# Kernel optimization log

Measured on AMD Instinct MI355X. Metric: run time of the kernel, lower is better.

Reference implementation:

```python
import jax, jax.numpy as jnp
import numpy as np
import math

H = 80; W = 80
FOVX = math.pi / 2.0; FOVY = math.pi / 2.0
TANX = math.tan(FOVX * 0.5); TANY = math.tan(FOVY * 0.5)
FOCAL_X = W / (2.0 * TANX); FOCAL_Y = H / (2.0 * TANY)
SCALE_MOD = 1.0
N_GAUSS = 4096; K_GEOM = 1024; K_SH = 1024

SH_C0 = 0.28209479177387814
SH_C1 = 0.4886025119029199
C2 = [1.0925484305920792, -1.0925484305920792, 0.31539156525252005, -1.0925484305920792, 0.5462742152960396]
C3 = [-0.5900435899266435, 2.890611442640554, -0.4570457994644658, 0.3731763325901154, -0.4570457994644658, 1.445305721320277, -0.5900435899266435]


def eval_sh3(sh, d):
    # sh: [N,16,3], d: [N,3] unit view directions -> clamped RGB [N,3]
    x, y, z = d[:, 0:1], d[:, 1:2], d[:, 2:3]
    xx, yy, zz = x * x, y * y, z * z
    xy, yz, xz = x * y, y * z, x * z
    res = (SH_C0 * sh[:, 0]
           - SH_C1 * y * sh[:, 1] + SH_C1 * z * sh[:, 2] - SH_C1 * x * sh[:, 3]
           + C2[0] * xy * sh[:, 4] + C2[1] * yz * sh[:, 5]
           + C2[2] * (2.0 * zz - xx - yy) * sh[:, 6]
           + C2[3] * xz * sh[:, 7] + C2[4] * (xx - yy) * sh[:, 8]
           + C3[0] * y * (3.0 * xx - yy) * sh[:, 9] + C3[1] * xy * z * sh[:, 10]
           + C3[2] * y * (4.0 * zz - xx - yy) * sh[:, 11]
           + C3[3] * z * (2.0 * zz - 3.0 * xx - 3.0 * yy) * sh[:, 12]
           + C3[4] * x * (4.0 * zz - xx - yy) * sh[:, 13]
           + C3[5] * z * (xx - yy) * sh[:, 14]
           + C3[6] * x * (xx - yy - 3.0 * zz) * sh[:, 15])
    return jnp.maximum(res + 0.5, 0.0)


def quat_to_rotmat(q):
    # q: [N,4] normalized (w,x,y,z) -> [N,3,3]
    w, x, y, z = q[:, 0], q[:, 1], q[:, 2], q[:, 3]
    r0 = jnp.stack([1 - 2 * (y * y + z * z), 2 * (x * y - w * z), 2 * (x * z + w * y)], -1)
    r1 = jnp.stack([2 * (x * y + w * z), 1 - 2 * (x * x + z * z), 2 * (y * z - w * x)], -1)
    r2 = jnp.stack([2 * (x * z - w * y), 2 * (y * z + w * x), 1 - 2 * (x * x + y * y)], -1)
    return jnp.stack([r0, r1, r2], axis=1)


def _forward(means3D, sh, sh_indices, g_indices, opacities, scales, scale_factors, rotations, extrinsic, bg):
    N = means3D.shape[0]
    # row-vector convention as in the torch wrapper: p_hom = [x,y,z,1] @ view
    R3 = extrinsic[:3, :3]; t3 = extrinsic[3, :3]
    p_view = means3D @ R3 + t3  # [N,3] camera space
    tx, ty, tz = p_view[:, 0], p_view[:, 1], p_view[:, 2]
    in_front = tz > 0.2  # near-plane cull as in CUDA kernel
    tz_s = jnp.where(in_front, tz, 1.0)
    # NDC (projection matrix reduces to x/(z tanx), y/(z tany)) then ndc2Pix
    gx = ((tx / (tz_s * TANX) + 1.0) * W - 1.0) * 0.5
    gy = ((ty / (tz_s * TANY) + 1.0) * H - 1.0) * 0.5
    # indexed 3D covariance: Sigma = R diag(s^2) R^T, codebook gathers
    s = scales[g_indices] * scale_factors * SCALE_MOD  # [N,3]
    q = rotations[g_indices]
    q = q / jnp.linalg.norm(q, axis=1, keepdims=True)
    Rm = quat_to_rotmat(q)
    cov3D = jnp.einsum('nij,nj,nkj->nik', Rm, s * s, Rm)
    # EWA splat: world->cam rotation is R3^T under row-vector storage
    Wm = R3.T
    cov_cam = jnp.einsum('ij,njk,lk->nil', Wm, cov3D, Wm)
    limx = 1.3 * TANX; limy = 1.3 * TANY
    txc = jnp.clip(tx / tz_s, -limx, limx) * tz_s
    tyc = jnp.clip(ty / tz_s, -limy, limy) * tz_s
    J = jnp.zeros((N, 2, 3), means3D.dtype)
    J = J.at[:, 0, 0].set(FOCAL_X / tz_s).at[:, 0, 2].set(-FOCAL_X * txc / (tz_s * tz_s))
    J = J.at[:, 1, 1].set(FOCAL_Y / tz_s).at[:, 1, 2].set(-FOCAL_Y * tyc / (tz_s * tz_s))
    cov2d = jnp.einsum('nij,njk,nlk->nil', J, cov_cam, J)
    a = cov2d[:, 0, 0] + 0.3; b = cov2d[:, 0, 1]; c = cov2d[:, 1, 1] + 0.3
    det = a * c - b * b
    valid = in_front & (det > 0)
    det_s = jnp.where(det != 0, det, 1.0)
    ca = c / det_s; cb = -b / det_s; cc = a / det_s  # conic
    mid = 0.5 * (a + c)
    lam1 = mid + jnp.sqrt(jnp.maximum(0.1, mid * mid - det))
    radii = jnp.where(valid, jnp.ceil(3.0 * jnp.sqrt(lam1)), 0.0).astype(jnp.int32)
    # SH -> RGB, view dir from camera position (extrinsic.inverse()[3,:3])
    campos = jnp.linalg.inv(extrinsic)[3, :3]
    dirs = means3D - campos
    dirs = dirs / jnp.linalg.norm(dirs, axis=1, keepdims=True)
    color = eval_sh3(sh[sh_indices], dirs)  # [N,3]
    # global front-to-back depth sort
    depth = jnp.where(valid, tz, jnp.inf)
    order = jnp.argsort(depth)
    gx_s, gy_s = gx[order], gy[order]
    ca_s, cb_s, cc_s = ca[order], cb[order], cc[order]
    op_s = opacities[order, 0]; col_s = color[order]; val_s = valid[order]
    # pixel grid (pixel centers at integer coords as in renderCUDA)
    ys, xs = jnp.meshgrid(jnp.arange(H, dtype=means3D.dtype), jnp.arange(W, dtype=means3D.dtype), indexing='ij')
    px = xs.reshape(-1); py = ys.reshape(-1)  # [P]
    dx = gx_s[None, :] - px[:, None]  # [P,N]
    dy = gy_s[None, :] - py[:, None]
    power = -0.5 * (ca_s * dx * dx + cc_s * dy * dy) - cb_s * dx * dy
    alpha = jnp.minimum(0.99, op_s[None, :] * jnp.exp(jnp.minimum(power, 0.0)))
    keep = (power <= 0.0) & val_s[None, :] & (alpha >= 1.0 / 255.0)
    alpha = jnp.where(keep, alpha, 0.0)
    om = 1.0 - alpha
    T_inc = jnp.cumprod(om, axis=1)
    inc = T_inc >= 1e-4  # early-termination prefix (T monotone)
    T_excl = jnp.concatenate([jnp.ones((px.shape[0], 1), om.dtype), T_inc[:, :-1]], axis=1)
    w = alpha * T_excl * inc
    T_final = jnp.prod(jnp.where(inc, om, 1.0), axis=1)
    out = w @ col_s + T_final[:, None] * bg[None, :]  # [P,3]
    color_img = jnp.transpose(out.reshape(H, W, 3), (2, 0, 1))  # [3,H,W]
    return color_img, radii


def setup_inputs() -> dict:
    key = jax.random.key(0)
    ks = jax.random.split(key, 9)
    xy = (jax.random.uniform(ks[0], (N_GAUSS, 2)) - 0.5) * 4.0
    z = jax.random.uniform(ks[1], (N_GAUSS, 1)) * 4.0 + 2.0
    means3D = jnp.concatenate([xy, z], axis=1)  # inside the view frustum
    sh = jax.random.normal(ks[2], (K_SH, 16, 3)) * 0.3
    sh_indices = jax.random.randint(ks[3], (N_GAUSS,), 0, K_SH)
    g_indices = jax.random.randint(ks[4], (N_GAUSS,), 0, K_GEOM)
    opacities = jax.random.uniform(ks[5], (N_GAUSS, 1), minval=0.1, maxval=0.99)
    scales = jax.random.uniform(ks[6], (K_GEOM, 3), minval=0.01, maxval=0.08)
    scale_factors = jax.random.uniform(ks[7], (N_GAUSS, 1), minval=0.5, maxval=1.5)
    rotations = jax.random.normal(ks[8], (K_GEOM, 4))
    extrinsic = jnp.eye(4, dtype=jnp.float32)
    bg = jnp.zeros((3,), jnp.float32)
    return dict(means3D=means3D, sh=sh, sh_indices=sh_indices, g_indices=g_indices,
                opacities=opacities, scales=scales, scale_factors=scale_factors,
                rotations=rotations, extrinsic=extrinsic, bg=bg)


def reference(means3D, sh, sh_indices, g_indices, opacities, scales, scale_factors, rotations, extrinsic, bg):
    return _forward(means3D, sh, sh_indices, g_indices, opacities, scales, scale_factors, rotations, extrinsic, bg)
```

## Files before the change

### kernel.cpp

```cpp
#include <hip/hip_runtime.h>
#include <math.h>

#define NG 4096
#define WI 80
#define HI 80
#define NPIX (WI*HI)
#define FOCAL 40.0f
#define LIM 1.3f
#define CAP 1536

#define SH_C0 0.28209479177387814f
#define SH_C1 0.4886025119029199f

#define U0_OFF 0
#define U1_OFF (64*1024)
#define U2_OFF (128*1024)
#define S0_OFF (192*1024)
#define B1_OFF (256*1024)
#define B2_OFF (320*1024)
#define B3_OFF (384*1024)
#define KD_OFF (400*1024)
#define RK_OFF (432*1024)

__global__ __launch_bounds__(256) void prep_k(
    const float* __restrict__ means, const float* __restrict__ sh,
    const int* __restrict__ shidx, const int* __restrict__ gidx,
    const float* __restrict__ opac, const float* __restrict__ scales,
    const float* __restrict__ sfac, const float* __restrict__ rots,
    const float* __restrict__ ext, char* __restrict__ wsb,
    float* __restrict__ radii_out)
{
  int i = blockIdx.x*blockDim.x + threadIdx.x;
  if (i >= NG) return;
  float e0=ext[0],  e1=ext[1],  e2=ext[2];
  float e4=ext[4],  e5=ext[5],  e6=ext[6];
  float e8=ext[8],  e9=ext[9],  e10=ext[10];
  float e12=ext[12], e13=ext[13], e14=ext[14];
  float m0=means[3*i+0], m1=means[3*i+1], m2=means[3*i+2];
  float tx = m0*e0 + m1*e4 + m2*e8  + e12;
  float ty = m0*e1 + m1*e5 + m2*e9  + e13;
  float tz = m0*e2 + m1*e6 + m2*e10 + e14;
  bool infront = tz > 0.2f;
  float tzs = infront ? tz : 1.0f;
  float inv_tzs = 1.0f / tzs;
  float gx = ((tx*inv_tzs + 1.0f)*WI - 1.0f)*0.5f;
  float gy = ((ty*inv_tzs + 1.0f)*HI - 1.0f)*0.5f;

  int gi = gidx[i];
  float sf = sfac[i];
  float s0 = scales[3*gi+0]*sf, s1 = scales[3*gi+1]*sf, s2 = scales[3*gi+2]*sf;
  float qw = rots[4*gi+0], qx = rots[4*gi+1], qy = rots[4*gi+2], qz = rots[4*gi+3];
  float qinv = rsqrtf(qw*qw+qx*qx+qy*qy+qz*qz);
  qw*=qinv; qx*=qinv; qy*=qinv; qz*=qinv;
  float r00 = 1.0f - 2.0f*(qy*qy+qz*qz);
  float r01 = 2.0f*(qx*qy - qw*qz);
  float r02 = 2.0f*(qx*qz + qw*qy);
  float r10 = 2.0f*(qx*qy + qw*qz);
  float r11 = 1.0f - 2.0f*(qx*qx+qz*qz);
  float r12 = 2.0f*(qy*qz - qw*qx);
  float r20 = 2.0f*(qx*qz - qw*qy);
  float r21 = 2.0f*(qy*qz + qw*qx);
  float r22 = 1.0f - 2.0f*(qx*qx+qy*qy);
  float v0 = s0*s0, v1 = s1*s1, v2 = s2*s2;
  float C00 = r00*r00*v0 + r01*r01*v1 + r02*r02*v2;
  float C01 = r00*r10*v0 + r01*r11*v1 + r02*r12*v2;
  float C02 = r00*r20*v0 + r01*r21*v1 + r02*r22*v2;
  float C11 = r10*r10*v0 + r11*r11*v1 + r12*r12*v2;
  float C12 = r10*r20*v0 + r11*r21*v1 + r12*r22*v2;
  float C22 = r20*r20*v0 + r21*r21*v1 + r22*r22*v2;
  float W0x=e0, W0y=e4, W0z=e8;
  float W1x=e1, W1y=e5, W1z=e9;
  float W2x=e2, W2y=e6, W2z=e10;
  float B00 = W0x*C00 + W0y*C01 + W0z*C02;
  float B01 = W0x*C01 + W0y*C11 + W0z*C12;
  float B02 = W0x*C02 + W0y*C12 + W0z*C22;
  float B10 = W1x*C00 + W1y*C01 + W1z*C02;
  float B11 = W1x*C01 + W1y*C11 + W1z*C12;
  float B12 = W1x*C02 + W1y*C12 + W1z*C22;
  float B20 = W2x*C00 + W2y*C01 + W2z*C02;
  float B21 = W2x*C01 + W2y*C11 + W2z*C12;
  float B22 = W2x*C02 + W2y*C12 + W2z*C22;
  float V00 = B00*W0x + B01*W0y + B02*W0z;
  float V02 = B00*W2x + B01*W2y + B02*W2z;
  float V01 = B00*W1x + B01*W1y + B02*W1z;
  float V11 = B10*W1x + B11*W1y + B12*W1z;
  float V12 = B10*W2x + B11*W2y + B12*W2z;
  float V22 = B20*W2x + B21*W2y + B22*W2z;
  float txz = tx*inv_tzs, tyz = ty*inv_tzs;
  float txc = fminf(fmaxf(txz, -LIM), LIM) * tzs;
  float tyc = fminf(fmaxf(tyz, -LIM), LIM) * tzs;
  float jx  = FOCAL*inv_tzs;
  float jy  = FOCAL*inv_tzs;
  float jz0 = -FOCAL*txc*inv_tzs*inv_tzs;
  float jz1 = -FOCAL*tyc*inv_tzs*inv_tzs;
  float c00 = jx*jx*V00 + 2.0f*jx*jz0*V02 + jz0*jz0*V22;
  float c01 = jx*jy*V01 + jx*jz1*V02 + jz0*jy*V12 + jz0*jz1*V22;
  float c11 = jy*jy*V11 + 2.0f*jy*jz1*V12 + jz1*jz1*V22;
  float a = c00 + 0.3f;
  float b = c01;
  float cf = c11 + 0.3f;
  float det = a*cf - b*b;
  bool valid = infront && (det > 0.0f);
  float dets = (det != 0.0f) ? det : 1.0f;
  float ca = cf/dets, cb = -b/dets, cc = a/dets;
  float mid = 0.5f*(a+cf);
  float lam1 = mid + sqrtf(fmaxf(0.1f, mid*mid - det));
  float radf = valid ? ceilf(3.0f*sqrtf(lam1)) : 0.0f;
  radii_out[i] = radf;

  float op = valid ? opac[i] : 0.0f;
  float L2 = 2.0f*fmaxf(0.0f, logf(255.0f*op));
  float rcx = valid ? sqrtf(L2*a)  + 0.01f : 0.0f;
  float rcy = valid ? sqrtf(L2*cf) + 0.01f : 0.0f;

  float cp0 = -(e12*e0 + e13*e1 + e14*e2);
  float cp1 = -(e12*e4 + e13*e5 + e14*e6);
  float cp2 = -(e12*e8 + e13*e9 + e14*e10);
  float dx0 = m0-cp0, dy0 = m1-cp1, dz0 = m2-cp2;
  float dn = rsqrtf(dx0*dx0+dy0*dy0+dz0*dz0);
  float x = dx0*dn, y = dy0*dn, z = dz0*dn;
  float xx=x*x, yy=y*y, zz=z*z;
  float xy=x*y, yz=y*z, xz=x*z;
  float bf[16];
  bf[0]  = SH_C0;
  bf[1]  = -SH_C1*y;
  bf[2]  =  SH_C1*z;
  bf[3]  = -SH_C1*x;
  bf[4]  =  1.0925484305920792f*xy;
  bf[5]  = -1.0925484305920792f*yz;
  bf[6]  =  0.31539156525252005f*(2.0f*zz-xx-yy);
  bf[7]  = -1.0925484305920792f*xz;
  bf[8]  =  0.5462742152960396f*(xx-yy);
  bf[9]  = -0.5900435899266435f*y*(3.0f*xx-yy);
  bf[10] =  2.890611442640554f*xy*z;
  bf[11] = -0.4570457994644658f*y*(4.0f*zz-xx-yy);
  bf[12] =  0.3731763325901154f*z*(2.0f*zz-3.0f*xx-3.0f*yy);
  bf[13] = -0.4570457994644658f*x*(4.0f*zz-xx-yy);
  bf[14] =  1.445305721320277f*z*(xx-yy);
  bf[15] = -0.5900435899266435f*x*(xx-yy-3.0f*zz);
  const float* S = sh + (long)shidx[i]*48;
  float cr=0.f, cg=0.f, cbl=0.f;
  #pragma unroll
  for (int j=0;j<16;j++) {
    float w = bf[j];
    cr  += w*S[j*3+0];
    cg  += w*S[j*3+1];
    cbl += w*S[j*3+2];
  }
  cr  = fmaxf(cr +0.5f, 0.0f);
  cg  = fmaxf(cg +0.5f, 0.0f);
  cbl = fmaxf(cbl+0.5f, 0.0f);

  float depth = infront ? tz : __builtin_inff();
  ((float4*)(wsb + U0_OFF))[i] = make_float4(gx, gy, rcx, rcy);
  ((float4*)(wsb + U1_OFF))[i] = make_float4(ca, cb, cc, op);
  ((float4*)(wsb + U2_OFF))[i] = make_float4(cr, cg, cbl, 0.0f);
  ((unsigned long long*)(wsb + KD_OFF))[i] =
      ((unsigned long long)__float_as_uint(depth) << 32) | (unsigned)i;
  ((int*)(wsb + RK_OFF))[i] = 0;
}

__global__ __launch_bounds__(256) void rank_k(const char* __restrict__ wsb,
                                              int* __restrict__ rank)
{
  const unsigned long long* kd = (const unsigned long long*)(wsb + KD_OFF);
  int tid = threadIdx.x;
  int i = blockIdx.x*256 + tid;
  unsigned long long ki = kd[i];
  int jb = blockIdx.y*256;
  int r = 0;
  #pragma unroll 8
  for (int jj = 0; jj < 256; ++jj) {
    unsigned long long kj = kd[jb + ((tid + jj) & 255)];
    r += (kj < ki);
  }
  atomicAdd(&rank[i], r);
}

__global__ __launch_bounds__(256) void scatter_k(char* __restrict__ wsb)
{
  int i = blockIdx.x*256 + threadIdx.x;
  int r = ((const int*)(wsb + RK_OFF))[i];
  float4 u0 = ((const float4*)(wsb + U0_OFF))[i];
  float4 u1 = ((const float4*)(wsb + U1_OFF))[i];
  float4 u2 = ((const float4*)(wsb + U2_OFF))[i];
  ((float4*)(wsb + S0_OFF))[r] = u0;
  ((float4*)(wsb + B1_OFF))[r] = make_float4(u0.x, u0.y, u1.x, u1.y);
  ((float4*)(wsb + B2_OFF))[r] = make_float4(u1.z, u1.w, u2.x, u2.y);
  ((float*) (wsb + B3_OFF))[r] = u2.z;
}

__global__ __launch_bounds__(512) void tile_k(const char* __restrict__ wsb,
                                              const float* __restrict__ bg,
                                              float* __restrict__ out)
{
  __shared__ int sidx[CAP];
  __shared__ int wcnt[2][8];
  __shared__ float pT[8][64], pR[8][64], pG[8][64], pB[8][64];
  const float4* S0 = (const float4*)(wsb + S0_OFF);
  const float4* B1 = (const float4*)(wsb + B1_OFF);
  const float4* B2 = (const float4*)(wsb + B2_OFF);
  const float*  B3 = (const float*) (wsb + B3_OFF);

  int tid = threadIdx.x;
  int wv = tid >> 6, lane = tid & 63;
  int tile = blockIdx.x;
  int x0 = (tile % 10) * 8, y0 = (tile / 10) * 8;
  float bx0 = (float)x0, bx1 = (float)(x0+7);
  float by0 = (float)y0, by1 = (float)(y0+7);

  int scnt = 0;
  for (int c = 0; c < NG/512; ++c) {
    int i = c*512 + tid;
    float4 v = S0[i];
    bool hit = (v.z > 0.0f) &&
               (v.x + v.z >= bx0) && (v.x - v.z <= bx1) &&
               (v.y + v.w >= by0) && (v.y - v.w <= by1);
    unsigned long long m = __ballot(hit);
    int par = c & 1;
    if (lane == 0) wcnt[par][wv] = __popcll(m);
    __syncthreads();
    int pre = 0, tot = 0;
    #pragma unroll
    for (int w = 0; w < 8; ++w) {
      int cw = wcnt[par][w];
      pre += (w < wv) ? cw : 0;
      tot += cw;
    }
    if (hit) {
      int pos = scnt + pre + __popcll(m & ((1ull<<lane)-1ull));
      if (pos < CAP) sidx[pos] = i;
    }
    scnt += tot;
  }
  __syncthreads();
  int cnt = scnt; if (cnt > CAP) cnt = CAP;

  float px = (float)(x0 + (lane & 7));
  float py = (float)(y0 + (lane >> 3));
  int seg = (cnt + 7) >> 3;
  int s0i = wv*seg;
  int s1i = s0i + seg; if (s1i > cnt) s1i = cnt;
  float T = 1.0f, ar = 0.f, ag = 0.f, ab = 0.f;
  for (int eb = s0i; eb < s1i; eb += 64) {
    int nn = s1i - eb; if (nn > 64) nn = 64;
    int myidx = (lane < nn) ? sidx[eb + lane] : 0;
    for (int c16 = 0; c16 < nn && __ballot(T >= 1e-4f); c16 += 16) {
      int ce = c16 + 16; if (ce > nn) ce = nn;
      #pragma unroll 4
      for (int e = c16; e < ce; ++e) {
        int g = __shfl(myidx, e, 64);
        float4 q1 = B1[g];
        float4 q2 = B2[g];
        float  b3 = B3[g];
        float dx = q1.x - px, dy = q1.y - py;
        float power = -0.5f*(q1.z*dx*dx + q2.x*dy*dy) - q1.w*dx*dy;
        float al = 0.0f;
        if (power <= 0.0f) {
          float av = fminf(0.99f, q2.y*__expf(power));
          if (av >= (1.0f/255.0f)) al = av;
        }
        float w = al*T;
        ar += w*q2.z; ag += w*q2.w; ab += w*b3;
        T *= 1.0f - al;
      }
    }
  }
  pT[wv][lane]=T; pR[wv][lane]=ar; pG[wv][lane]=ag; pB[wv][lane]=ab;
  __syncthreads();

  if (tid < 64) {
    float Tg = 1.0f, r = 0.f, g2 = 0.f, b2 = 0.f;
    #pragma unroll
    for (int w = 0; w < 8; ++w) {
      r  += Tg*pR[w][tid];
      g2 += Tg*pG[w][tid];
      b2 += Tg*pB[w][tid];
      Tg *= pT[w][tid];
    }
    int p = (y0 + (tid>>3))*WI + (x0 + (tid&7));
    out[0*NPIX+p] = r  + Tg*bg[0];
    out[1*NPIX+p] = g2 + Tg*bg[1];
    out[2*NPIX+p] = b2 + Tg*bg[2];
  }
}

extern "C" void kernel_launch(void* const* d_in, const int* in_sizes, int n_in,
                              void* d_out, int out_size, void* d_ws, size_t ws_size,
                              hipStream_t stream) {
  const float* means  = (const float*)d_in[0];
  const float* sh     = (const float*)d_in[1];
  const int*   shidx  = (const int*)  d_in[2];
  const int*   gidx   = (const int*)  d_in[3];
  const float* opac   = (const float*)d_in[4];
  const float* scales = (const float*)d_in[5];
  const float* sfac   = (const float*)d_in[6];
  const float* rots   = (const float*)d_in[7];
  const float* ext    = (const float*)d_in[8];
  const float* bg     = (const float*)d_in[9];
  float* out = (float*)d_out;
  char* wsb = (char*)d_ws;

  prep_k<<<NG/256, 256, 0, stream>>>(means, sh, shidx, gidx, opac, scales, sfac,
                                     rots, ext, wsb, out + 3*NPIX);
  dim3 rg(NG/256, NG/256);
  rank_k<<<rg, 256, 0, stream>>>(wsb, (int*)(wsb + RK_OFF));
  scatter_k<<<NG/256, 256, 0, stream>>>(wsb);
  tile_k<<<100, 512, 0, stream>>>(wsb, bg, out);
}
```

Baseline: 115.2 us.

## Split depth range into partitions per tile and merge with combine kernel

The tile rasterizer now launches 4x more blocks, each handling one quarter of the depth-sorted Gaussians for a tile, and writes partial transmittance and colour that a new combine kernel composites in order. Per-Gaussian data is copied into shared memory during culling, and the inner loop broadcasts parameters with readlane instead of shfl plus global loads. The aim is to fill more of the GPU than 100 blocks can and to cut global-memory latency in the blend loop. The cost is an extra kernel launch, a partial-results buffer, and early termination that can no longer cross partitions.

```diff
diff --git a/kernel.cpp b/kernel.cpp
--- a/kernel.cpp
+++ b/kernel.cpp
@@ -7,7 +7,8 @@
 #define NPIX (WI*HI)
 #define FOCAL 40.0f
 #define LIM 1.3f
-#define CAP 1536
+#define NPART 4
+#define RANGE (NG/NPART)
 
 #define SH_C0 0.28209479177387814f
 #define SH_C1 0.4886025119029199f
@@ -21,6 +22,11 @@
 #define B3_OFF (384*1024)
 #define KD_OFF (400*1024)
 #define RK_OFF (432*1024)
+#define PP_OFF (448*1024)
+
+__device__ inline float rdlane(float v, int l) {
+  return __uint_as_float(__builtin_amdgcn_readlane(__float_as_uint(v), l));
+}
 
 __global__ __launch_bounds__(256) void prep_k(
     const float* __restrict__ means, const float* __restrict__ sh,
@@ -191,12 +197,13 @@
 }
 
 __global__ __launch_bounds__(512) void tile_k(const char* __restrict__ wsb,
-                                              const float* __restrict__ bg,
-                                              float* __restrict__ out)
-{
-  __shared__ int sidx[CAP];
-  __shared__ int wcnt[2][8];
-  __shared__ float pT[8][64], pR[8][64], pG[8][64], pB[8][64];
+                                              float4* __restrict__ pp)
+{
+  __shared__ float4 sb1[RANGE];
+  __shared__ float4 sb2[RANGE];
+  __shared__ float  sb3[RANGE];
+  __shared__ int    wcnt[2][8];
+  __shared__ float  pT[8][64], pR[8][64], pG[8][64], pB[8][64];
   const float4* S0 = (const float4*)(wsb + S0_OFF);
   const float4* B1 = (const float4*)(wsb + B1_OFF);
   const float4* B2 = (const float4*)(wsb + B2_OFF);
@@ -204,14 +211,17 @@
 
   int tid = threadIdx.x;
   int wv = tid >> 6, lane = tid & 63;
-  int tile = blockIdx.x;
+  int part = blockIdx.x / 100;
+  int tile = blockIdx.x % 100;
+  int base = part * RANGE;
   int x0 = (tile % 10) * 8, y0 = (tile / 10) * 8;
   float bx0 = (float)x0, bx1 = (float)(x0+7);
   float by0 = (float)y0, by1 = (float)(y0+7);
 
   int scnt = 0;
-  for (int c = 0; c < NG/512; ++c) {
-    int i = c*512 + tid;
+  #pragma unroll
+  for (int c = 0; c < RANGE/512; ++c) {
+    int i = base + c*512 + tid;
     float4 v = S0[i];
     bool hit = (v.z > 0.0f) &&
                (v.x + v.z >= bx0) && (v.x - v.z <= bx1) &&
@@ -229,12 +239,14 @@
     }
     if (hit) {
       int pos = scnt + pre + __popcll(m & ((1ull<<lane)-1ull));
-      if (pos < CAP) sidx[pos] = i;
+      sb1[pos] = B1[i];
+      sb2[pos] = B2[i];
+      sb3[pos] = B3[i];
     }
     scnt += tot;
   }
   __syncthreads();
-  int cnt = scnt; if (cnt > CAP) cnt = CAP;
+  int cnt = scnt;
 
   float px = (float)(x0 + (lane & 7));
   float py = (float)(y0 + (lane >> 3));
@@ -244,24 +256,26 @@
   float T = 1.0f, ar = 0.f, ag = 0.f, ab = 0.f;
   for (int eb = s0i; eb < s1i; eb += 64) {
     int nn = s1i - eb; if (nn > 64) nn = 64;
-    int myidx = (lane < nn) ? sidx[eb + lane] : 0;
+    float4 q1 = (lane < nn) ? sb1[eb+lane] : make_float4(0.f,0.f,0.f,0.f);
+    float4 q2 = (lane < nn) ? sb2[eb+lane] : make_float4(0.f,0.f,0.f,0.f);
+    float  r3 = (lane < nn) ? sb3[eb+lane] : 0.f;
     for (int c16 = 0; c16 < nn && __ballot(T >= 1e-4f); c16 += 16) {
       int ce = c16 + 16; if (ce > nn) ce = nn;
-      #pragma unroll 4
       for (int e = c16; e < ce; ++e) {
-        int g = __shfl(myidx, e, 64);
-        float4 q1 = B1[g];
-        float4 q2 = B2[g];
-        float  b3 = B3[g];
-        float dx = q1.x - px, dy = q1.y - py;
-        float power = -0.5f*(q1.z*dx*dx + q2.x*dy*dy) - q1.w*dx*dy;
+        float gxe = rdlane(q1.x, e), gye = rdlane(q1.y, e);
+        float cae = rdlane(q1.z, e), cbe = rdlane(q1.w, e);
+        float cce = rdlane(q2.x, e), ope = rdlane(q2.y, e);
+        float cre = rdlane(q2.z, e), cge = rdlane(q2.w, e);
+        float cble = rdlane(r3, e);
+        float dx = gxe - px, dy = gye - py;
+        float power = -0.5f*(cae*dx*dx + cce*dy*dy) - cbe*dx*dy;
         float al = 0.0f;
         if (power <= 0.0f) {
-          float av = fminf(0.99f, q2.y*__expf(power));
+          float av = fminf(0.99f, ope*__expf(power));
           if (av >= (1.0f/255.0f)) al = av;
         }
         float w = al*T;
-        ar += w*q2.z; ag += w*q2.w; ab += w*b3;
+        ar += w*cre; ag += w*cge; ab += w*cble;
         T *= 1.0f - al;
       }
     }
@@ -279,10 +293,25 @@
       Tg *= pT[w][tid];
     }
     int p = (y0 + (tid>>3))*WI + (x0 + (tid&7));
-    out[0*NPIX+p] = r  + Tg*bg[0];
-    out[1*NPIX+p] = g2 + Tg*bg[1];
-    out[2*NPIX+p] = b2 + Tg*bg[2];
-  }
+    pp[part*NPIX + p] = make_float4(Tg, r, g2, b2);
+  }
+}
+
+__global__ __launch_bounds__(256) void combine_k(const float4* __restrict__ pp,
+                                                 const float* __restrict__ bg,
+                                                 float* __restrict__ out)
+{
+  int p = blockIdx.x*256 + threadIdx.x;
+  float T = 1.0f, r = 0.f, g = 0.f, b = 0.f;
+  #pragma unroll
+  for (int part = 0; part < NPART; ++part) {
+    float4 q = pp[part*NPIX + p];
+    r += T*q.y; g += T*q.z; b += T*q.w;
+    T *= q.x;
+  }
+  out[0*NPIX+p] = r + T*bg[0];
+  out[1*NPIX+p] = g + T*bg[1];
+  out[2*NPIX+p] = b + T*bg[2];
 }
 
 extern "C" void kernel_launch(void* const* d_in, const int* in_sizes, int n_in,
@@ -300,11 +329,13 @@
   const float* bg     = (const float*)d_in[9];
   float* out = (float*)d_out;
   char* wsb = (char*)d_ws;
+  float4* pp = (float4*)(wsb + PP_OFF);
 
   prep_k<<<NG/256, 256, 0, stream>>>(means, sh, shidx, gidx, opac, scales, sfac,
                                      rots, ext, wsb, out + 3*NPIX);
   dim3 rg(NG/256, NG/256);
   rank_k<<<rg, 256, 0, stream>>>(wsb, (int*)(wsb + RK_OFF));
   scatter_k<<<NG/256, 256, 0, stream>>>(wsb);
-  tile_k<<<100, 512, 0, stream>>>(wsb, bg, out);
-}
+  tile_k<<<100*NPART, 512, 0, stream>>>(wsb, pp);
+  combine_k<<<NPIX/256, 256, 0, stream>>>(pp, bg, out);
+}
```

Measured after the change: 95.17 us. 17.4% less time.
